# Performance work log

Measured on AMD Instinct MI355X. Metric: run time of the kernel, lower is better.

## Reference

```python
import jax, jax.numpy as jnp
import numpy as np

N = 100000   # nodes
E = 1600000  # directed edges
F_IN = 256
H = 128
C = 64

def setup_inputs() -> dict:
    key = jax.random.key(0)
    k = jax.random.split(key, 6)
    x = jax.random.normal(k[0], (N, F_IN), dtype=jnp.float32)
    edge_index = jax.random.randint(k[1], (2, E), 0, N)
    def glorot(kk, fan_in, fan_out):
        s = jnp.sqrt(6.0 / (fan_in + fan_out)).astype(jnp.float32)
        return jax.random.uniform(kk, (fan_in, fan_out), jnp.float32, -s, s)
    W0 = glorot(k[2], F_IN, H)
    W1 = glorot(k[3], H, H)
    W2 = glorot(k[4], H, H)
    W3 = glorot(k[5], H, C)
    return {"x": x, "edge_index": edge_index, "W0": W0, "W1": W1, "W2": W2, "W3": W3}

def _gcn_norm(edge_index, num_nodes):
    # add self loops, compute symmetric normalization 1/sqrt(deg_i * deg_j)
    loops = jnp.arange(num_nodes, dtype=edge_index.dtype)
    row = jnp.concatenate([edge_index[0], loops])
    col = jnp.concatenate([edge_index[1], loops])
    deg = jax.ops.segment_sum(jnp.ones_like(row, dtype=jnp.float32), row, num_segments=num_nodes)
    dinv = jnp.where(deg > 0, jax.lax.rsqrt(deg), 0.0)
    norm = dinv[row] * dinv[col]  # [E+N]
    return row, col, norm

def _gcn_conv(h, W, row, col, norm, num_nodes):
    h = h @ W                      # [N, d_out]
    msg = h[col] * norm[:, None]   # gather + scale, [E+N, d_out]
    return jax.ops.segment_sum(msg, row, num_segments=num_nodes)

def _feat_corr_metric(h):
    # torch_corr(x.t()): Pearson correlation across feature columns -> [d, d]
    hc = h - jnp.mean(h, axis=0, keepdims=True)
    cov = hc.T @ hc                                 # [d, d]
    sd = jnp.sqrt(jnp.clip(jnp.diag(cov), 1e-12))
    corr = cov / (sd[:, None] * sd[None, :])
    n = corr.shape[0]
    upper = jnp.abs(jnp.triu(corr, 1))
    return upper.sum() / (n * (n - 1) / 2)

def reference(x, edge_index, W0, W1, W2, W3):
    row, col, norm = _gcn_norm(edge_index, N)
    Ws = [W0, W1, W2, W3]
    num_layers = len(Ws)
    h = x
    corr_2 = jnp.float32(0.0)
    corr = jnp.float32(0.0)
    for i, W in enumerate(Ws):
        h = _gcn_conv(h, W, row, col, norm, N)  # type_norm='None' -> bn is identity; eval -> dropout identity
        if i == num_layers - 2:
            corr_2 = _feat_corr_metric(h)
        if i == num_layers - 1:
            corr = _feat_corr_metric(h)
        if i != num_layers - 1:
            h = jax.nn.relu(h)
    return h, corr_2, corr
```

## Files before the change

### kernel.cpp

```cpp
#include <hip/hip_runtime.h>

#define NN 100000
#define FIN 256
#define HD 128
#define CD 64
#define RG 8
#define RSZ 12500
#define CH 32

typedef __attribute__((ext_vector_type(8))) short bf16x8;
typedef __attribute__((ext_vector_type(4))) float f32x4;
typedef __attribute__((ext_vector_type(2))) float f32x2;
typedef __attribute__((ext_vector_type(4))) unsigned int u32x4;

__device__ __forceinline__ float bf2f(unsigned int u16) {
    union { unsigned int u; float f; } v;
    v.u = (u16 & 0xffffu) << 16;
    return v.f;
}
__device__ __forceinline__ unsigned short f2bf(float f) {
    union { float f; unsigned int u; } v;
    v.f = f;
    unsigned int u = v.u + 0x7fffu + ((v.u >> 16) & 1u);
    return (unsigned short)(u >> 16);
}

__global__ void k_detect(const unsigned short* __restrict__ x, int* __restrict__ flag) {
    __shared__ int s[256];
    int t = threadIdx.x;
    int c = 0;
    for (int i = t; i < 16384; i += 256) {
        unsigned int e = (x[2 * i] >> 7) & 0xFF;
        c += (e >= 112 && e <= 134) ? 1 : 0;
    }
    s[t] = c;
    __syncthreads();
    for (int off = 128; off > 0; off >>= 1) {
        if (t < off) s[t] += s[t + off];
        __syncthreads();
    }
    if (t == 0) *flag = (s[0] > 8192) ? 1 : 0;
}

template <int K, int COLS>
__global__ void k_packW(const void* __restrict__ src, unsigned short* __restrict__ dst,
                        const int* __restrict__ dflag) {
    constexpr int CT = COLS / 16;
    int i = blockIdx.x * 256 + threadIdx.x;
    if (i >= K * COLS) return;
    int j = i & 7;
    int lane = (i >> 3) & 63;
    int rest = i >> 9;
    int ct = rest % CT;
    int kt = rest / CT;
    int k = kt * 32 + (lane >> 4) * 8 + j;
    int c = ct * 16 + (lane & 15);
    int si = k * COLS + c;
    dst[i] = (*dflag) ? ((const unsigned short*)src)[si] : f2bf(((const float*)src)[si]);
}

__global__ __launch_bounds__(1024) void k_histL(const int* __restrict__ row,
                                                int* __restrict__ partial, int E) {
    __shared__ int lbin[RSZ];
    int r = blockIdx.x & (RG - 1);
    int c = blockIdx.x >> 3;
    int lo = r * RSZ;
    for (int i = threadIdx.x; i < RSZ; i += 1024) lbin[i] = 0;
    __syncthreads();
    int cs = (E + CH - 1) / CH;
    int e0 = c * cs;
    int e1 = e0 + cs;
    if (e1 > E) e1 = E;
    for (int e = e0 + threadIdx.x; e < e1; e += 1024) {
        unsigned int rr = (unsigned int)row[e];
        if (rr >= NN) rr = 0;
        unsigned int d = rr - (unsigned int)lo;
        if (d < RSZ) atomicAdd(&lbin[d], 1);
    }
    __syncthreads();
    int* pc = partial + (size_t)c * NN + lo;
    for (int i = threadIdx.x; i < RSZ; i += 1024) pc[i] = lbin[i];
}

__global__ __launch_bounds__(256) void k_histpre(int* __restrict__ partial,
                                                 int* __restrict__ cnt, int n) {
    int i = blockIdx.x * 256 + threadIdx.x;
    if (i >= n) return;
    int run = 0;
#pragma unroll
    for (int c = 0; c < CH; c++) {
        int t = partial[(size_t)c * NN + i];
        partial[(size_t)c * NN + i] = run;
        run += t;
    }
    cnt[i] = run;
}

__global__ void k_scan_a(const int* __restrict__ cnt, int* __restrict__ bsum, int n) {
    __shared__ int s[256];
    int i = blockIdx.x * 256 + threadIdx.x;
    s[threadIdx.x] = (i < n) ? cnt[i] : 0;
    __syncthreads();
    for (int off = 128; off > 0; off >>= 1) {
        if (threadIdx.x < off) s[threadIdx.x] += s[threadIdx.x + off];
        __syncthreads();
    }
    if (threadIdx.x == 0) bsum[blockIdx.x] = s[0];
}

__global__ void k_scan_b(int* bsum, int nchunks) {
    __shared__ int s[512];
    int t = threadIdx.x;
    int v = (t < nchunks) ? bsum[t] : 0;
    s[t] = v;
    __syncthreads();
    for (int off = 1; off < 512; off <<= 1) {
        int x = (t >= off) ? s[t - off] : 0;
        __syncthreads();
        s[t] += x;
        __syncthreads();
    }
    if (t < nchunks) bsum[t] = s[t] - v;
}

__global__ void k_scan_c(const int* __restrict__ cnt, const int* __restrict__ bsum,
                         int* __restrict__ offs, int n) {
    __shared__ int s[256];
    int t = threadIdx.x;
    int i = blockIdx.x * 256 + t;
    int v = (i < n) ? cnt[i] : 0;
    s[t] = v;
    __syncthreads();
    for (int off = 1; off < 256; off <<= 1) {
        int x = (t >= off) ? s[t - off] : 0;
        __syncthreads();
        s[t] += x;
        __syncthreads();
    }
    if (i < n) offs[i] = bsum[blockIdx.x] + s[t] - v;
}

__global__ __launch_bounds__(1024) void k_scatL(const int* __restrict__ row,
                                                const int* __restrict__ col,
                                                const int* __restrict__ offs,
                                                const int* __restrict__ partial,
                                                int* __restrict__ colS, int E) {
    __shared__ int lcur[RSZ];
    int r = blockIdx.x & (RG - 1);
    int c = blockIdx.x >> 3;
    int lo = r * RSZ;
    const int* pc = partial + (size_t)c * NN + lo;
    const int* po = offs + lo;
    for (int i = threadIdx.x; i < RSZ; i += 1024) lcur[i] = po[i] + pc[i];
    __syncthreads();
    int cs = (E + CH - 1) / CH;
    int e0 = c * cs;
    int e1 = e0 + cs;
    if (e1 > E) e1 = E;
    for (int e = e0 + threadIdx.x; e < e1; e += 1024) {
        unsigned int rr = (unsigned int)row[e];
        if (rr >= NN) rr = 0;
        unsigned int d = rr - (unsigned int)lo;
        if (d < RSZ) {
            unsigned int cc = (unsigned int)col[e];
            if (cc >= NN) cc = 0;
            int p = atomicAdd(&lcur[d], 1);
            colS[p] = (int)cc;
        }
    }
}

__global__ void k_dinv(const int* __restrict__ cnt, float* __restrict__ dinv, int n) {
    int i = blockIdx.x * 256 + threadIdx.x;
    if (i < n) dinv[i] = rsqrtf((float)(cnt[i] + 1));
}

template <int K, int COLS, bool RELU, int AMODE>
__global__ __launch_bounds__(256) void k_gemm(const void* __restrict__ Av,
                                              const unsigned short* __restrict__ Wp,
                                              const float* __restrict__ dinv,
                                              unsigned short* __restrict__ G, int nrows,
                                              const int* __restrict__ dflag) {
    constexpr int CT = COLS / 16;
    constexpr int KT = K / 32;
    constexpr bool SW = (K * COLS * 2) <= 32768;
    __shared__ unsigned short tile[4][16][136];
    __shared__ unsigned short ldsW[SW ? (K * COLS) : 8];

    int t = threadIdx.x;
    int wave = t >> 6, lane = t & 63;
    int quad = lane >> 4, m = lane & 15;
    int r0 = blockIdx.x * 64 + wave * 16;
    int arow = r0 + m;
    bool rowok = arow < nrows;
    bool abf = (AMODE == 0) || (*dflag != 0);

    const unsigned short* Ab = (const unsigned short*)Av;
    const float* Af = (const float*)Av;

    if constexpr (SW) {
        const u32x4* src = (const u32x4*)Wp;
        u32x4* dst = (u32x4*)ldsW;
        for (int i = t; i < K * COLS / 8; i += 256) dst[i] = src[i];
        __syncthreads();
    }

    bf16x8 afr[KT];
#pragma unroll
    for (int kt = 0; kt < KT; kt++) afr[kt] = (bf16x8)0;
    if (rowok) {
        if (abf) {
#pragma unroll
            for (int kt = 0; kt < KT; kt++)
                afr[kt] = *(const bf16x8*)(Ab + (size_t)arow * K + kt * 32 + quad * 8);
            if constexpr (RELU) {
#pragma unroll
                for (int kt = 0; kt < KT; kt++) {
#pragma unroll
                    for (int j = 0; j < 8; j++) {
                        unsigned short u = (unsigned short)afr[kt][j];
                        afr[kt][j] = (u & 0x8000u) ? (short)0 : (short)u;
                    }
                }
            }
        } else {
#pragma unroll
            for (int kt = 0; kt < KT; kt++) {
                float4 f0 = *(const float4*)(Af + (size_t)arow * K + kt * 32 + quad * 8);
                float4 f1 = *(const float4*)(Af + (size_t)arow * K + kt * 32 + quad * 8 + 4);
                afr[kt][0] = (short)f2bf(f0.x); afr[kt][1] = (short)f2bf(f0.y);
                afr[kt][2] = (short)f2bf(f0.z); afr[kt][3] = (short)f2bf(f0.w);
                afr[kt][4] = (short)f2bf(f1.x); afr[kt][5] = (short)f2bf(f1.y);
                afr[kt][6] = (short)f2bf(f1.z); afr[kt][7] = (short)f2bf(f1.w);
            }
        }
    }

    f32x4 acc[CT];
#pragma unroll
    for (int ct = 0; ct < CT; ct++) acc[ct] = (f32x4){0.f, 0.f, 0.f, 0.f};

#pragma unroll
    for (int kt = 0; kt < KT; kt++) {
#pragma unroll
        for (int ct = 0; ct < CT; ct++) {
            bf16x8 bfrag;
            if constexpr (SW)
                bfrag = *(const bf16x8*)&ldsW[(((size_t)kt * CT + ct) * 64 + lane) * 8];
            else
                bfrag = *(const bf16x8*)(Wp + (((size_t)kt * CT + ct) * 64 + lane) * 8);
            acc[ct] = __builtin_amdgcn_mfma_f32_16x16x32_bf16(afr[kt], bfrag, acc[ct], 0, 0, 0);
        }
    }

    float dv[4];
#pragma unroll
    for (int rg = 0; rg < 4; rg++) {
        int gr = r0 + quad * 4 + rg;
        dv[rg] = dinv[gr < nrows ? gr : 0];
    }
#pragma unroll
    for (int ct = 0; ct < CT; ct++) {
#pragma unroll
        for (int rg = 0; rg < 4; rg++)
            tile[wave][quad * 4 + rg][ct * 16 + m] = f2bf(acc[ct][rg] * dv[rg]);
    }
    int srow = lane >> 2;
    int grow = r0 + srow;
    if (grow < nrows) {
        constexpr int CH2 = COLS / 32;
#pragma unroll
        for (int j8 = 0; j8 < CH2; j8++) {
            int c = (lane & 3) * 8 + j8 * 32;
            uint4 v = *(const uint4*)&tile[wave][srow][c];
            *(uint4*)(G + (size_t)grow * COLS + c) = v;
        }
    }
}

__device__ __forceinline__ f32x2 bfpair(unsigned int u) {
    union { unsigned int u; float f; } lo, hi;
    lo.u = u << 16;
    hi.u = u & 0xffff0000u;
    return (f32x2){lo.f, hi.f};
}
__device__ __forceinline__ void acc8p(f32x2* a, uint4 u) {
    a[0] += bfpair(u.x);
    a[1] += bfpair(u.y);
    a[2] += bfpair(u.z);
    a[3] += bfpair(u.w);
}

template <int D, bool RELU, bool FINAL>
__global__ __launch_bounds__(256) void k_agg(const unsigned short* __restrict__ g,
                                             const int* __restrict__ colS,
                                             const int* __restrict__ offs,
                                             const int* __restrict__ cnt,
                                             const float* __restrict__ dinv,
                                             unsigned short* __restrict__ obf,
                                             void* __restrict__ oraw,
                                             const int* __restrict__ dflag, int n) {
    constexpr int GRP = (D == 128) ? 4 : 8;
    constexpr int LPR = 64 / GRP;
    int lane = threadIdx.x & 63;
    int node = blockIdx.x * 4 + (threadIdx.x >> 6);
    if (node >= n) return;
    int gq = lane / LPR;
    int li = lane % LPR;
    int start = offs[node];
    int deg = cnt[node];

    f32x2 a[4];
#pragma unroll
    for (int i = 0; i < 4; i++) a[i] = (f32x2){0.f, 0.f};

    if (gq == 0) {
        uint4 u = *(const uint4*)(g + (size_t)node * D + li * 8);
        acc8p(a, u);
    }

    for (int base = 0; base < deg; base += 64) {
        int rem = deg - base;
        int nb = rem < 64 ? rem : 64;
        int cidx = 0;
        if (lane < nb) cidx = colS[start + base + lane];
        int j = 0;
        if constexpr (D == 128) {
            for (; j + 8 <= nb; j += 8) {
                int ca = __shfl(cidx, j + gq);
                int cb = __shfl(cidx, j + 4 + gq);
                uint4 ua = *(const uint4*)(g + (size_t)ca * D + li * 8);
                uint4 ub = *(const uint4*)(g + (size_t)cb * D + li * 8);
                acc8p(a, ua);
                acc8p(a, ub);
            }
            for (; j < nb; j += 4) {
                int jj = j + gq;
                int cc = __shfl(cidx, jj < nb ? jj : (nb - 1));
                if (jj < nb) {
                    uint4 u = *(const uint4*)(g + (size_t)cc * D + li * 8);
                    acc8p(a, u);
                }
            }
        } else {
            for (; j + 8 <= nb; j += 8) {
                int cc = __shfl(cidx, j + gq);
                uint4 u = *(const uint4*)(g + (size_t)cc * D + li * 8);
                acc8p(a, u);
            }
            for (; j < nb; j += 8) {
                int jj = j + gq;
                int cc = __shfl(cidx, jj < nb ? jj : (nb - 1));
                if (jj < nb) {
                    uint4 u = *(const uint4*)(g + (size_t)cc * D + li * 8);
                    acc8p(a, u);
                }
            }
        }
    }

#pragma unroll
    for (int i = 0; i < 4; i++) {
        if constexpr (D == 64) {
            a[i].x += __shfl_xor(a[i].x, 8);
            a[i].y += __shfl_xor(a[i].y, 8);
        }
        a[i].x += __shfl_xor(a[i].x, 16);
        a[i].y += __shfl_xor(a[i].y, 16);
        a[i].x += __shfl_xor(a[i].x, 32);
        a[i].y += __shfl_xor(a[i].y, 32);
    }

    float s = dinv[node];
    f32x2 sv = {s, s};
#pragma unroll
    for (int i = 0; i < 4; i++) {
        a[i] *= sv;
        if constexpr (RELU)
            a[i] = (f32x2){fmaxf(a[i].x, 0.f), fmaxf(a[i].y, 0.f)};
    }

    if (gq == 0) {
        uint4 o;
        o.x = (unsigned int)f2bf(a[0].x) | ((unsigned int)f2bf(a[0].y) << 16);
        o.y = (unsigned int)f2bf(a[1].x) | ((unsigned int)f2bf(a[1].y) << 16);
        o.z = (unsigned int)f2bf(a[2].x) | ((unsigned int)f2bf(a[2].y) << 16);
        o.w = (unsigned int)f2bf(a[3].x) | ((unsigned int)f2bf(a[3].y) << 16);
        *(uint4*)(obf + (size_t)node * D + li * 8) = o;
        if constexpr (FINAL) {
            if (*dflag) {
                *(uint4*)((unsigned short*)oraw + (size_t)node * D + li * 8) = o;
            } else {
                float* op = (float*)oraw + (size_t)node * D + li * 8;
                *(float4*)op = (float4){a[0].x, a[0].y, a[1].x, a[1].y};
                *(float4*)(op + 4) = (float4){a[2].x, a[2].y, a[3].x, a[3].y};
            }
        }
    }
}

template <int D>
__global__ __launch_bounds__(256) void k_colsum(const unsigned short* __restrict__ in,
                                                float* __restrict__ colsum, int n) {
    constexpr int CG = D / 8;
    constexpr int RPB = 256 / CG;
    __shared__ float red[RPB][D];
    int t = threadIdx.x;
    int cg = t % CG, r0 = t / CG;
    int c0 = cg * 8;
    float a[8];
#pragma unroll
    for (int i = 0; i < 8; i++) a[i] = 0.f;
    for (int r = blockIdx.x * RPB + r0; r < n; r += gridDim.x * RPB) {
        bf16x8 u = *(const bf16x8*)(in + (size_t)r * D + c0);
#pragma unroll
        for (int i = 0; i < 8; i++) a[i] += bf2f((unsigned short)u[i]);
    }
#pragma unroll
    for (int i = 0; i < 8; i++) red[r0][c0 + i] = a[i];
    __syncthreads();
    if (t < D) {
        float s = 0.f;
#pragma unroll
        for (int r = 0; r < RPB; r++) s += red[r][t];
        atomicAdd(&colsum[t], s);
    }
}

template <int D>
__global__ __launch_bounds__(256) void k_cov2(const unsigned short* __restrict__ in,
                                              const float* __restrict__ colsum,
                                              float* __restrict__ part, int n, int nblocks) {
    constexpr int CT = D / 16;
    constexpr int TPW = (D == 128) ? 2 : 1;
    constexpr int CG = D / 8;
    __shared__ unsigned int lds32[D * 16];
    __shared__ float smean[D];

    int t = threadIdx.x;
    int wave = t >> 6, lane = t & 63;
    int quad = lane >> 4, m = lane & 15;

    if (t < D) smean[t] = colsum[t] * (1.0f / (float)NN);
    __syncthreads();

    f32x4 accA[CT], accB[CT];
#pragma unroll
    for (int tc = 0; tc < CT; tc++) {
        accA[tc] = (f32x4){0.f, 0.f, 0.f, 0.f};
        accB[tc] = (f32x4){0.f, 0.f, 0.f, 0.f};
    }

    bool stager = (t < 16 * CG);
    int kp = stager ? (t / CG) : 0;
    int c0 = stager ? ((t % CG) * 8) : 0;
    int slot = (((kp >> 2) + (c0 >> 3)) & 3) * 4 + (kp & 3);
    float sm[8];
#pragma unroll
    for (int i = 0; i < 8; i++) sm[i] = smean[c0 + i];

    int ca0 = (wave * TPW) * 16 + m;
    int ga0 = (quad + (ca0 >> 3)) & 3;
    int ca1 = ca0 + 16;
    int ga1 = (quad + (ca1 >> 3)) & 3;

    int nchunks = (n + 31) / 32;
    for (int ch = blockIdx.x; ch < nchunks; ch += nblocks) {
        int k0 = ch * 32;
        if (stager) {
            int k = k0 + 2 * kp;
            bf16x8 u0 = (bf16x8)0, u1 = (bf16x8)0;
            bool ok0 = (k < n), ok1 = (k + 1 < n);
            if (ok0) u0 = *(const bf16x8*)(in + (size_t)k * D + c0);
            if (ok1) u1 = *(const bf16x8*)(in + (size_t)(k + 1) * D + c0);
#pragma unroll
            for (int i = 0; i < 8; i++) {
                float a = ok0 ? (bf2f((unsigned short)u0[i]) - sm[i]) : 0.f;
                float b = ok1 ? (bf2f((unsigned short)u1[i]) - sm[i]) : 0.f;
                lds32[(c0 + i) * 16 + slot] = (unsigned int)f2bf(a) | ((unsigned int)f2bf(b) << 16);
            }
        }
        __syncthreads();

        bf16x8 bfr[CT];
#pragma unroll
        for (int tc = 0; tc < CT; tc++) {
            int c = tc * 16 + m;
            int grp = (quad + (c >> 3)) & 3;
            bfr[tc] = *(const bf16x8*)&lds32[c * 16 + grp * 4];
        }
        bf16x8 afr0 = *(const bf16x8*)&lds32[ca0 * 16 + ga0 * 4];
#pragma unroll
        for (int tc = 0; tc < CT; tc++)
            accA[tc] = __builtin_amdgcn_mfma_f32_16x16x32_bf16(afr0, bfr[tc], accA[tc], 0, 0, 0);
        if constexpr (TPW == 2) {
            bf16x8 afr1 = *(const bf16x8*)&lds32[ca1 * 16 + ga1 * 4];
#pragma unroll
            for (int tc = 0; tc < CT; tc++)
                accB[tc] = __builtin_amdgcn_mfma_f32_16x16x32_bf16(afr1, bfr[tc], accB[tc], 0, 0, 0);
        }
        __syncthreads();
    }

    float* p = part + (size_t)blockIdx.x * D * D;
    int tr0 = wave * TPW;
#pragma unroll
    for (int tc = 0; tc < CT; tc++) {
#pragma unroll
        for (int rg = 0; rg < 4; rg++) {
            int cj = tc * 16 + m;
            p[(tr0 * 16 + quad * 4 + rg) * D + cj] = accA[tc][rg];
            if constexpr (TPW == 2)
                p[((tr0 + 1) * 16 + quad * 4 + rg) * D + cj] = accB[tc][rg];
        }
    }
}

template <int D>
__global__ __launch_bounds__(256) void k_covred(const float* __restrict__ part,
                                                float* __restrict__ cov, int nblocks) {
    __shared__ float red[256];
    int t = threadIdx.x;
    int il = t & 63;
    int bs = t >> 6;
    int idx = blockIdx.x * 64 + il;
    float s = 0.f;
    for (int b = bs; b < nblocks; b += 4)
        s += part[(size_t)b * D * D + idx];
    red[t] = s;
    __syncthreads();
    if (t < 64)
        cov[idx] = red[t] + red[t + 64] + red[t + 128] + red[t + 192];
}

template <int D>
__global__ __launch_bounds__(256) void k_fin(const float* __restrict__ cov,
                                             void* __restrict__ out, long long idx,
                                             const int* __restrict__ dflag) {
    __shared__ float sd[D];
    __shared__ float red[256];
    int t = threadIdx.x;
    if (t < D) sd[t] = sqrtf(fmaxf(cov[t * D + t], 1e-12f));
    __syncthreads();
    float s = 0.f;
    for (int i2 = t; i2 < D * D; i2 += 256) {
        int i = i2 / D, j = i2 % D;
        if (j > i) s += fabsf(cov[i2] / (sd[i] * sd[j]));
    }
    red[t] = s;
    __syncthreads();
    for (int off = 128; off > 0; off >>= 1) {
        if (t < off) red[t] += red[t + off];
        __syncthreads();
    }
    if (t == 0) {
        float v = red[0] / (float)(D * (D - 1) / 2);
        if (*dflag) ((unsigned short*)out)[idx] = f2bf(v);
        else        ((float*)out)[idx] = v;
    }
}

extern "C" void kernel_launch(void* const* d_in, const int* in_sizes, int n_in,
                              void* d_out, int out_size, void* d_ws, size_t ws_size,
                              hipStream_t stream) {
    const void* x = d_in[0];
    const int* ei = (const int*)d_in[1];

    int E = in_sizes[1] / 2;
    const int* row = ei;
    const int* col = ei + E;

    char* w = (char*)d_ws;
    auto carve = [&](size_t bytes) {
        void* p = (void*)w;
        w += (bytes + 255) & ~(size_t)255;
        return p;
    };
    int* cnt = (int*)carve((size_t)NN * 4);
    int* offs = (int*)carve((size_t)NN * 4);
    int* bsum = (int*)carve(512 * 4);
    int* colS = (int*)carve((size_t)E * 4);
    float* dinv = (float*)carve((size_t)NN * 4);
    float* colsum = (float*)carve(HD * 4);
    float* covs = (float*)carve(HD * HD * 4);
    int* dflag = (int*)carve(256);
    unsigned short* wc = (unsigned short*)carve((size_t)(FIN * HD + HD * HD * 2 + HD * CD) * 2);
    unsigned short* bufA = (unsigned short*)carve((size_t)NN * HD * 2);
    unsigned short* bufB = (unsigned short*)carve((size_t)NN * HD * 2);

    unsigned short* wc0 = wc;
    unsigned short* wc1 = wc + FIN * HD;
    unsigned short* wc2 = wc1 + HD * HD;
    unsigned short* wc3 = wc2 + HD * HD;

    float* part = (float*)bufB;
    int* chp = (int*)bufB;
    const int NBC = 250;

    int nchunks = (NN + 255) / 256;
    int GB = (NN + 63) / 64;

    k_detect<<<1, 256, 0, stream>>>((const unsigned short*)x, dflag);
    k_packW<256, 128><<<(FIN * HD) / 256, 256, 0, stream>>>(d_in[2], wc0, dflag);
    k_packW<128, 128><<<(HD * HD) / 256, 256, 0, stream>>>(d_in[3], wc1, dflag);
    k_packW<128, 128><<<(HD * HD) / 256, 256, 0, stream>>>(d_in[4], wc2, dflag);
    k_packW<128, 64><<<(HD * CD) / 256, 256, 0, stream>>>(d_in[5], wc3, dflag);

    k_histL<<<RG * CH, 1024, 0, stream>>>(row, chp, E);
    k_histpre<<<nchunks, 256, 0, stream>>>(chp, cnt, NN);
    k_scan_a<<<nchunks, 256, 0, stream>>>(cnt, bsum, NN);
    k_scan_b<<<1, 512, 0, stream>>>(bsum, nchunks);
    k_scan_c<<<nchunks, 256, 0, stream>>>(cnt, bsum, offs, NN);
    k_scatL<<<RG * CH, 1024, 0, stream>>>(row, col, offs, chp, colS, E);
    k_dinv<<<nchunks, 256, 0, stream>>>(cnt, dinv, NN);

    k_gemm<256, 128, false, 2><<<GB, 256, 0, stream>>>(x, wc0, dinv, bufB, NN, dflag);
    k_agg<128, true, false><<<NN / 4, 256, 0, stream>>>(bufB, colS, offs, cnt, dinv, bufA, nullptr, dflag, NN);
    k_gemm<128, 128, false, 0><<<GB, 256, 0, stream>>>(bufA, wc1, dinv, bufB, NN, dflag);
    k_agg<128, true, false><<<NN / 4, 256, 0, stream>>>(bufB, colS, offs, cnt, dinv, bufA, nullptr, dflag, NN);
    k_gemm<128, 128, false, 0><<<GB, 256, 0, stream>>>(bufA, wc2, dinv, bufB, NN, dflag);
    k_agg<128, false, false><<<NN / 4, 256, 0, stream>>>(bufB, colS, offs, cnt, dinv, bufA, nullptr, dflag, NN);

    hipMemsetAsync(colsum, 0, HD * 4, stream);
    k_colsum<128><<<64, 256, 0, stream>>>(bufA, colsum, NN);
    k_cov2<128><<<NBC, 256, 0, stream>>>(bufA, colsum, part, NN, NBC);
    k_covred<128><<<(HD * HD) / 64, 256, 0, stream>>>(part, covs, NBC);
    k_fin<128><<<1, 256, 0, stream>>>(covs, d_out, (long long)NN * CD, dflag);

    k_gemm<128, 64, true, 0><<<GB, 256, 0, stream>>>(bufA, wc3, dinv, bufB, NN, dflag);
    k_agg<64, false, true><<<NN / 4, 256, 0, stream>>>(bufB, colS, offs, cnt, dinv, bufA, d_out, dflag, NN);

    hipMemsetAsync(colsum, 0, HD * 4, stream);
    k_colsum<64><<<64, 256, 0, stream>>>(bufA, colsum, NN);
    k_cov2<64><<<NBC, 256, 0, stream>>>(bufA, colsum, part, NN, NBC);
    k_covred<64><<<(CD * CD) / 64, 256, 0, stream>>>(part, covs, NBC);
    k_fin<64><<<1, 256, 0, stream>>>(covs, d_out, (long long)NN * CD + 1, dflag);
}
```

Before: 703.1 us.

## Fuse aggregation with following GEMM for middle GCN layers via reordering

Uses the identity A(hW) = (Ah)W for layers 1 and 2. Each node's neighbours are aggregated first at width 128 and written to a shared-memory tile, then an in-block MFMA multiplies that tile by the weight matrix, so the separate GEMM launches and their global round trips go away. The previous aggregation now applies a second dinv scale (PSCALE) so that the pre-scaled inputs the fused kernel expects are ready. The gather width stays 128 and each block holds only 16 nodes, so load balance across blocks and the extra bf16 rounding points may change performance and accuracy.

```diff
diff --git a/kernel.cpp b/kernel.cpp
--- a/kernel.cpp
+++ b/kernel.cpp
@@ -291,7 +291,7 @@
     a[3] += bfpair(u.w);
 }
 
-template <int D, bool RELU, bool FINAL>
+template <int D, bool RELU, bool PSCALE, bool FINAL>
 __global__ __launch_bounds__(256) void k_agg(const unsigned short* __restrict__ g,
                                              const int* __restrict__ colS,
                                              const int* __restrict__ offs,
@@ -378,6 +378,7 @@
         a[i] *= sv;
         if constexpr (RELU)
             a[i] = (f32x2){fmaxf(a[i].x, 0.f), fmaxf(a[i].y, 0.f)};
+        if constexpr (PSCALE) a[i] *= sv;
     }
 
     if (gq == 0) {
@@ -397,6 +398,118 @@
             }
         }
     }
+}
+
+__device__ __forceinline__ void acc8s(float* a, uint4 u) {
+    a[0] += bf2f(u.x); a[1] += bf2f(u.x >> 16);
+    a[2] += bf2f(u.y); a[3] += bf2f(u.y >> 16);
+    a[4] += bf2f(u.z); a[5] += bf2f(u.z >> 16);
+    a[6] += bf2f(u.w); a[7] += bf2f(u.w >> 16);
+}
+
+template <bool PSCALE>
+__global__ __launch_bounds__(256) void k_fused(const unsigned short* __restrict__ s,
+                                               const unsigned short* __restrict__ Wp,
+                                               const int* __restrict__ colS,
+                                               const int* __restrict__ offs,
+                                               const int* __restrict__ cnt,
+                                               const float* __restrict__ dinv,
+                                               unsigned short* __restrict__ out) {
+    constexpr int CT = 8;
+    __shared__ unsigned short tile[16][136];
+    __shared__ unsigned short otile[16][136];
+    int t = threadIdx.x;
+    int wave = t >> 6, lane = t & 63;
+    int quad = lane >> 4, m = lane & 15;
+    int gq = lane >> 4;
+    int li = lane & 15;
+    int n0 = blockIdx.x * 16;
+
+    for (int k = 0; k < 4; k++) {
+        int node = n0 + wave * 4 + k;
+        int start = offs[node];
+        int deg = cnt[node];
+        float a[8];
+#pragma unroll
+        for (int i = 0; i < 8; i++) a[i] = 0.f;
+        if (gq == 0) {
+            uint4 u = *(const uint4*)(s + (size_t)node * 128 + li * 8);
+            acc8s(a, u);
+        }
+        for (int base = 0; base < deg; base += 64) {
+            int rem = deg - base;
+            int nb = rem < 64 ? rem : 64;
+            int cidx = 0;
+            if (lane < nb) cidx = colS[start + base + lane];
+            int j = 0;
+            for (; j + 8 <= nb; j += 8) {
+                int ca = __shfl(cidx, j + gq);
+                int cb = __shfl(cidx, j + 4 + gq);
+                uint4 ua = *(const uint4*)(s + (size_t)ca * 128 + li * 8);
+                uint4 ub = *(const uint4*)(s + (size_t)cb * 128 + li * 8);
+                acc8s(a, ua);
+                acc8s(a, ub);
+            }
+            for (; j < nb; j += 4) {
+                int jj = j + gq;
+                int cc = __shfl(cidx, jj < nb ? jj : (nb - 1));
+                if (jj < nb) {
+                    uint4 u = *(const uint4*)(s + (size_t)cc * 128 + li * 8);
+                    acc8s(a, u);
+                }
+            }
+        }
+#pragma unroll
+        for (int i = 0; i < 8; i++) {
+            a[i] += __shfl_xor(a[i], 16);
+            a[i] += __shfl_xor(a[i], 32);
+        }
+        if (gq == 0) {
+            uint4 o;
+            o.x = (unsigned int)f2bf(a[0]) | ((unsigned int)f2bf(a[1]) << 16);
+            o.y = (unsigned int)f2bf(a[2]) | ((unsigned int)f2bf(a[3]) << 16);
+            o.z = (unsigned int)f2bf(a[4]) | ((unsigned int)f2bf(a[5]) << 16);
+            o.w = (unsigned int)f2bf(a[6]) | ((unsigned int)f2bf(a[7]) << 16);
+            *(uint4*)&tile[wave * 4 + k][li * 8] = o;
+        }
+    }
+    __syncthreads();
+
+    bf16x8 afr[4];
+#pragma unroll
+    for (int kt = 0; kt < 4; kt++)
+        afr[kt] = *(const bf16x8*)&tile[m][kt * 32 + quad * 8];
+
+    f32x4 acc0 = (f32x4){0.f, 0.f, 0.f, 0.f};
+    f32x4 acc1 = (f32x4){0.f, 0.f, 0.f, 0.f};
+    int ct0 = 2 * wave, ct1 = 2 * wave + 1;
+#pragma unroll
+    for (int kt = 0; kt < 4; kt++) {
+        bf16x8 b0 = *(const bf16x8*)(Wp + (((size_t)kt * CT + ct0) * 64 + lane) * 8);
+        bf16x8 b1 = *(const bf16x8*)(Wp + (((size_t)kt * CT + ct1) * 64 + lane) * 8);
+        acc0 = __builtin_amdgcn_mfma_f32_16x16x32_bf16(afr[kt], b0, acc0, 0, 0, 0);
+        acc1 = __builtin_amdgcn_mfma_f32_16x16x32_bf16(afr[kt], b1, acc1, 0, 0, 0);
+    }
+
+    float dv[4];
+#pragma unroll
+    for (int rg = 0; rg < 4; rg++) dv[rg] = dinv[n0 + quad * 4 + rg];
+#pragma unroll
+    for (int rg = 0; rg < 4; rg++) {
+        float y0 = acc0[rg] * dv[rg];
+        float y1 = acc1[rg] * dv[rg];
+        if constexpr (PSCALE) {
+            y0 = dv[rg] * fmaxf(y0, 0.f);
+            y1 = dv[rg] * fmaxf(y1, 0.f);
+        }
+        otile[quad * 4 + rg][ct0 * 16 + m] = f2bf(y0);
+        otile[quad * 4 + rg][ct1 * 16 + m] = f2bf(y1);
+    }
+    __syncthreads();
+
+    int row = t >> 4, ci = (t & 15) * 8;
+    uint4 v = *(const uint4*)&otile[row][ci];
+    *(uint4*)(out + (size_t)(n0 + row) * 128 + ci) = v;
 }
 
 template <int D>
@@ -615,11 +728,10 @@
     k_dinv<<<nchunks, 256, 0, stream>>>(cnt, dinv, NN);
 
     k_gemm<256, 128, false, 2><<<GB, 256, 0, stream>>>(x, wc0, dinv, bufB, NN, dflag);
-    k_agg<128, true, false><<<NN / 4, 256, 0, stream>>>(bufB, colS, offs, cnt, dinv, bufA, nullptr, dflag, NN);
-    k_gemm<128, 128, false, 0><<<GB, 256, 0, stream>>>(bufA, wc1, dinv, bufB, NN, dflag);
-    k_agg<128, true, false><<<NN / 4, 256, 0, stream>>>(bufB, colS, offs, cnt, dinv, bufA, nullptr, dflag, NN);
-    k_gemm<128, 128, false, 0><<<GB, 256, 0, stream>>>(bufA, wc2, dinv, bufB, NN, dflag);
-    k_agg<128, false, false><<<NN / 4, 256, 0, stream>>>(bufB, colS, offs, cnt, dinv, bufA, nullptr, dflag, NN);
+    k_agg<128, true, true, false><<<NN / 4, 256, 0, stream>>>(bufB, colS, offs, cnt, dinv, bufA, nullptr, dflag, NN);
+
+    k_fused<true><<<NN / 16, 256, 0, stream>>>(bufA, wc1, colS, offs, cnt, dinv, bufB);
+    k_fused<false><<<NN / 16, 256, 0, stream>>>(bufB, wc2, colS, offs, cnt, dinv, bufA);
 
     hipMemsetAsync(colsum, 0, HD * 4, stream);
     k_colsum<128><<<64, 256, 0, stream>>>(bufA, colsum, NN);
@@ -628,7 +740,7 @@
     k_fin<128><<<1, 256, 0, stream>>>(covs, d_out, (long long)NN * CD, dflag);
 
     k_gemm<128, 64, true, 0><<<GB, 256, 0, stream>>>(bufA, wc3, dinv, bufB, NN, dflag);
-    k_agg<64, false, true><<<NN / 4, 256, 0, stream>>>(bufB, colS, offs, cnt, dinv, bufA, d_out, dflag, NN);
+    k_agg<64, false, false, true><<<NN / 4, 256, 0, stream>>>(bufB, colS, offs, cnt, dinv, bufA, d_out, dflag, NN);
 
     hipMemsetAsync(colsum, 0, HD * 4, stream);
     k_colsum<64><<<64, 256, 0, stream>>>(bufA, colsum, NN);
```

After: 683.3 us. 2.8% less time.
